# Kernel tuning notes

Hardware: AMD Instinct MI355X
Metric: run time of the kernel (lower is better)

## Reference

```python
import jax, jax.numpy as jnp
import numpy as np

NLAT, NLON = 361, 720
LMAX = NLAT               # equiangular grid: lmax = nlat
MMAX = NLON // 2 + 1      # mmax = nlon//2 + 1
B, C = 1, 128


def _precompute_legpoly(mmax, lmax, t, csphase=True):
    """Associated Legendre vandermonde P_l^m(cos t), orthonormal, inverse=True
    (norm factor 1 for 'ortho'). Shape [mmax, lmax, nlat]. Setup-time numpy only."""
    x = np.cos(t)
    nmax = max(mmax, lmax)
    vdm = np.zeros((nmax, nmax, len(x)))
    vdm[0, 0] = np.sqrt(1.0 / (4.0 * np.pi))
    for l in range(1, nmax):
        vdm[l - 1, l] = np.sqrt(2 * l + 1) * x * vdm[l - 1, l - 1]
        vdm[l, l] = np.sqrt((2 * l + 1) * (1 + x) * (1 - x) / (2 * l)) * vdm[l - 1, l - 1]
    for l in range(2, nmax):
        for m in range(l - 1):
            a = np.sqrt((2 * l - 1) / (l - m) * (2 * l + 1) / (l + m))
            b = np.sqrt((l + m - 1) / (l - m) * (2 * l + 1) / (2 * l - 3) * (l - m - 1) / (l + m))
            vdm[m, l] = a * x * vdm[m, l - 1] - b * vdm[m, l - 2]
    vdm = vdm[:mmax, :lmax]
    if csphase:
        vdm[1::2] *= -1.0  # Condon-Shortley phase on odd m
    return vdm


def setup_inputs() -> dict:
    key = jax.random.key(0)
    # spherical harmonic coefficients as real view: [B, C, lmax, mmax, 2]
    x_real = jax.random.normal(key, (B, C, LMAX, MMAX, 2), dtype=jnp.float32)
    # equiangular (Clenshaw-Curtiss) colatitudes, t = flip(arccos(cos(pi*j/(n-1))))
    t = np.pi * np.arange(NLAT) / (NLAT - 1)
    pct = jnp.asarray(_precompute_legpoly(MMAX, LMAX, t), dtype=jnp.float32)  # [mmax, lmax, nlat]
    return {"x_real": x_real, "pct": pct}


def reference(x_real, pct):
    # single-device case: comm sizes == 1, all distributed transposes are identity
    # and nlatpad == nlonpad == 0.
    # per-m triangular Legendre contraction over l (torch einsum '...lmr,mlk->...kmr')
    xs = jnp.einsum('bclmr,mlk->bckmr', x_real, pct)        # [B, C, nlat, mmax, 2]
    xc = jax.lax.complex(xs[..., 0], xs[..., 1])            # [B, C, nlat, mmax]
    # inverse real FFT along longitude, norm='forward' (no 1/n scaling on inverse)
    out = jnp.fft.irfft(xc, n=NLON, axis=-1, norm='forward')  # [B, C, nlat, nlon]
    return out.astype(x_real.dtype)
```

## Files before the change

kernel.cpp:

```cpp
#include <hip/hip_runtime.h>
#include <cstddef>

#define CC   128
#define LDIM 361
#define MDIM 361
#define KDIM 361
#define NLON 720
#define LP   384
#define KP   384
#define MRP  736
#define NP   768
#define CK   (CC*KDIM)
#define CR   (2*CC)

typedef __attribute__((ext_vector_type(8))) short short8;
typedef __attribute__((ext_vector_type(4))) float floatx4;

__device__ __forceinline__ unsigned short f2bf(float f) {
    union { float f; unsigned u; } v; v.f = f;
    unsigned u = v.u;
    u += 0x7fffu + ((u >> 16) & 1u);
    return (unsigned short)(u >> 16);
}

__device__ __forceinline__ void async_copy16(const void* g, void* l) {
    __builtin_amdgcn_global_load_lds(
        (const __attribute__((address_space(1))) void*)g,
        (__attribute__((address_space(3))) void*)l, 16, 0, 0);
}

__device__ __forceinline__ int xcd_swz(int id, int P) {
    int x = id & 7, g = id >> 3;
    int q = P >> 3, r = P & 7;
    int start = (x < r) ? x * (q + 1) : r * (q + 1) + (x - r) * q;
    return start + g;
}

__global__ void sht_gen_T(unsigned short* __restrict__ Tp) {
    int idx = blockIdx.x * 256 + threadIdx.x;
    if (idx >= NP * MRP) return;
    int n = idx / MRP, mr = idx - n * MRP;
    float v = 0.f;
    if (n < NLON && mr < 2 * MDIM) {
        int m = mr >> 1, im = mr & 1;
        if (m == 0)            v = im ? 0.f : 1.f;
        else if (m == MDIM-1)  v = im ? 0.f : ((n & 1) ? -1.f : 1.f);
        else {
            int ph = (m * n) % NLON;
            float ang = (float)ph * (float)(3.14159265358979323846 / 360.0);
            v = im ? (-2.f * sinf(ang)) : (2.f * cosf(ang));
        }
    }
    Tp[idx] = f2bf(v);
}

__global__ __launch_bounds__(256)
void sht_prep_x(const float* __restrict__ x, unsigned short* __restrict__ xA) {
    __shared__ float tp[2][64 * 33 + 4];
    const int mt = blockIdx.x;
    const int lt = blockIdx.y;
    const int c  = blockIdx.z;
    const int t  = threadIdx.x;

    #pragma unroll
    for (int u = 0; u < 8; ++u) {
        int p  = t + 256 * u;
        int li = p >> 5, mi = p & 31;
        int l = lt * 64 + li, m = mt * 32 + mi;
        float2 v = make_float2(0.f, 0.f);
        if (l < LDIM && m < MDIM)
            v = *(const float2*)(x + ((size_t)(c * LDIM + l) * MDIM + m) * 2);
        tp[0][li * 33 + mi] = v.x;
        tp[1][li * 33 + mi] = v.y;
    }
    __syncthreads();

    #pragma unroll
    for (int u = 0; u < 2; ++u) {
        int s  = t + 256 * u;
        int mi = s >> 4, rr = (s >> 3) & 1, lo = (s & 7) * 8;
        int m = mt * 32 + mi;
        if (m >= MDIM) continue;
        const float* pl = tp[rr];
        short8 h;
        #pragma unroll
        for (int e = 0; e < 8; ++e)
            h[e] = (short)f2bf(pl[(lo + e) * 33 + mi]);
        *(short8*)(xA + ((size_t)m * CR + 2 * c + rr) * LP + lt * 64 + lo) = h;
    }
}

__global__ __launch_bounds__(256)
void sht_prep_pct(const float* __restrict__ pct, unsigned short* __restrict__ pctT) {
    __shared__ float tile[32][129];
    const int m  = blockIdx.y;
    const int bx = blockIdx.x;
    const int kt = bx % 3, lt = bx / 3;
    const int l0 = lt * 32, k0 = kt * 128;
    const int t  = threadIdx.x;

    const int kk = t & 127, lw = t >> 7;
    #pragma unroll
    for (int u = 0; u < 16; ++u) {
        int li = lw + 2 * u;
        int l = l0 + li, k = k0 + kk;
        float v = 0.f;
        if (l < LDIM && k < KDIM)
            v = pct[((size_t)m * LDIM + l) * KDIM + k];
        tile[li][kk] = v;
    }
    __syncthreads();

    #pragma unroll
    for (int u = 0; u < 2; ++u) {
        int s = t + 256 * u;
        int ko = s >> 2, lo = (s & 3) * 8;
        short8 h;
        #pragma unroll
        for (int e = 0; e < 8; ++e)
            h[e] = (short)f2bf(tile[lo + e][ko]);
        *(short8*)(pctT + ((size_t)m * KP + k0 + ko) * LP + l0 + lo) = h;
    }
}

__global__ __launch_bounds__(512)
void sht_stageA2(const unsigned short* __restrict__ pctT, const unsigned short* __restrict__ xA,
                 unsigned short* __restrict__ xs) {
    __shared__ unsigned short As[128 * 32];
    __shared__ unsigned short Bs[384 * 32];

    const int p   = xcd_swz(blockIdx.x, 2 * MDIM);
    const int m   = p >> 1, ct = p & 1;
    const int c0  = ct * 128;
    const int t   = threadIdx.x;
    const int w   = t >> 6, L = t & 63;
    const int wr  = w & 1, wc = w >> 1;
    const int lane15 = L & 15, quad = L >> 4;
    const int arr = t >> 2, alq = t & 3;

    const unsigned short* xAm = xA + (size_t)m * CR * LP;
    const unsigned short* pTm = pctT + (size_t)m * KP * LP;

    floatx4 acc[4][6] = {};

    for (int kb = 0; kb < LP; kb += 32) {
        async_copy16(xAm + (size_t)(c0 + arr) * LP + kb + alq * 8,
                     As + (size_t)(w * 64) * 8);
        #pragma unroll
        for (int u = 0; u < 3; ++u) {
            int s = u * 512 + t;
            int rr = s >> 2, lq = s & 3;
            async_copy16(pTm + (size_t)rr * LP + kb + lq * 8,
                         Bs + (size_t)(u * 512 + w * 64) * 8);
        }
        __syncthreads();

        short8 af[4], bf[6];
        #pragma unroll
        for (int i = 0; i < 4; ++i)
            af[i] = *(const short8*)&As[((wr * 64 + i * 16 + lane15) * 4 + quad) * 8];
        #pragma unroll
        for (int j = 0; j < 6; ++j)
            bf[j] = *(const short8*)&Bs[((wc * 96 + j * 16 + lane15) * 4 + quad) * 8];
        #pragma unroll
        for (int i = 0; i < 4; ++i)
            #pragma unroll
            for (int j = 0; j < 6; ++j)
                acc[i][j] = __builtin_amdgcn_mfma_f32_16x16x32_bf16(af[i], bf[j], acc[i][j], 0, 0, 0);
        __syncthreads();
    }

    #pragma unroll
    for (int j = 0; j < 6; ++j) {
        int k = wc * 96 + j * 16 + lane15;
        if (k >= KDIM) continue;
        #pragma unroll
        for (int i = 0; i < 4; ++i) {
            #pragma unroll
            for (int eh = 0; eh < 2; ++eh) {
                int cr = c0 + wr * 64 + i * 16 + quad * 4 + eh * 2;
                int c  = cr >> 1;
                unsigned pack = (unsigned)f2bf(acc[i][j][eh * 2]) |
                                ((unsigned)f2bf(acc[i][j][eh * 2 + 1]) << 16);
                *(unsigned*)(xs + (size_t)(c * KDIM + k) * MRP + 2 * m) = pack;
            }
        }
    }
}

__global__ __launch_bounds__(256)
void sht_stageA(const float* __restrict__ pct, const unsigned short* __restrict__ xA,
                unsigned short* __restrict__ xs) {
    __shared__ unsigned short As[128 * 32];
    __shared__ unsigned short Bs[32 * 130];

    const int m   = blockIdx.y;
    const int ct  = blockIdx.x & 1;
    const int kt  = blockIdx.x >> 1;
    const int c0  = ct * 128;
    const int n0  = kt * 128;
    const int t   = threadIdx.x;
    const int w   = t >> 6, L = t & 63;
    const int wr  = w & 1, wc = w >> 1;
    const int lane15 = L & 15, quad = L >> 4;
    const int bl = t >> 3, bkq = t & 7;

    const unsigned short* xAm = xA + (size_t)m * CR * LP;
    const float* pctm = pct + (size_t)m * LDIM * KDIM;

    floatx4 acc[4][4] = {};

    for (int kb = 0; kb < LP; kb += 32) {
        #pragma unroll
        for (int i = 0; i < 2; ++i) {
            int s = w * 128 + i * 64 + L;
            int cr = s >> 2, lq = s & 3;
            async_copy16(xAm + (size_t)(c0 + cr) * LP + kb + lq * 8,
                         As + (size_t)(w * 128 + i * 64) * 8);
        }
        {
            int l = kb + bl;
            bool lok = (l < LDIM);
            const float* prow = pctm + (size_t)l * KDIM;
            #pragma unroll
            for (int u = 0; u < 4; ++u) {
                int kc = n0 + u * 32 + bkq * 4;
                float f0 = (lok && kc + 0 < KDIM) ? prow[kc + 0] : 0.f;
                float f1 = (lok && kc + 1 < KDIM) ? prow[kc + 1] : 0.f;
                float f2 = (lok && kc + 2 < KDIM) ? prow[kc + 2] : 0.f;
                float f3 = (lok && kc + 3 < KDIM) ? prow[kc + 3] : 0.f;
                unsigned* bp = (unsigned*)&Bs[bl * 130 + u * 32 + bkq * 4];
                bp[0] = (unsigned)f2bf(f0) | ((unsigned)f2bf(f1) << 16);
                bp[1] = (unsigned)f2bf(f2) | ((unsigned)f2bf(f3) << 16);
            }
        }
        __syncthreads();

        short8 af[4];
        #pragma unroll
        for (int i = 0; i < 4; ++i) {
            int row = wr * 64 + i * 16 + lane15;
            af[i] = *(const short8*)&As[(row * 4 + quad) * 8];
        }
        #pragma unroll
        for (int jf = 0; jf < 4; ++jf) {
            int col = wc * 64 + jf * 16 + lane15;
            short8 bf;
            #pragma unroll
            for (int j = 0; j < 8; ++j)
                bf[j] = (short)Bs[(quad * 8 + j) * 130 + col];
            #pragma unroll
            for (int i = 0; i < 4; ++i)
                acc[i][jf] = __builtin_amdgcn_mfma_f32_16x16x32_bf16(af[i], bf, acc[i][jf], 0, 0, 0);
        }
        __syncthreads();
    }

    #pragma unroll
    for (int i = 0; i < 4; ++i) {
        #pragma unroll
        for (int jf = 0; jf < 4; ++jf) {
            int k = n0 + wc * 64 + jf * 16 + lane15;
            if (k >= KDIM) continue;
            #pragma unroll
            for (int eh = 0; eh < 2; ++eh) {
                int cr = c0 + wr * 64 + i * 16 + quad * 4 + eh * 2;
                int c  = cr >> 1;
                unsigned pack = (unsigned)f2bf(acc[i][jf][eh * 2]) |
                                ((unsigned)f2bf(acc[i][jf][eh * 2 + 1]) << 16);
                *(unsigned*)(xs + (size_t)(c * KDIM + k) * MRP + 2 * m) = pack;
            }
        }
    }
}

__global__ __launch_bounds__(512)
void sht_stageB2(const unsigned short* __restrict__ xs, const unsigned short* __restrict__ Tp,
                 float* __restrict__ out) {
    __shared__ unsigned short As[128 * 32];
    __shared__ unsigned short Bs[384 * 32];

    const int p   = xcd_swz(blockIdx.x, 2 * MDIM);
    const int ckt = p >> 1, nt = p & 1;
    const int ck0 = ckt * 128, n0 = nt * 384;
    const int t   = threadIdx.x;
    const int w   = t >> 6, L = t & 63;
    const int wr  = w & 1, wc = w >> 1;
    const int lane15 = L & 15, quad = L >> 4;
    const int arr = t >> 2, alq = t & 3;

    floatx4 acc[4][6] = {};

    for (int kb = 0; kb < MRP; kb += 32) {
        async_copy16(xs + (size_t)(ck0 + arr) * MRP + kb + alq * 8,
                     As + (size_t)(w * 64) * 8);
        #pragma unroll
        for (int u = 0; u < 3; ++u) {
            int s = u * 512 + t;
            int rr = s >> 2, lq = s & 3;
            async_copy16(Tp + (size_t)(n0 + rr) * MRP + kb + lq * 8,
                         Bs + (size_t)(u * 512 + w * 64) * 8);
        }
        __syncthreads();

        short8 af[4], bf[6];
        #pragma unroll
        for (int i = 0; i < 4; ++i)
            af[i] = *(const short8*)&As[((wr * 64 + i * 16 + lane15) * 4 + quad) * 8];
        #pragma unroll
        for (int j = 0; j < 6; ++j)
            bf[j] = *(const short8*)&Bs[((wc * 96 + j * 16 + lane15) * 4 + quad) * 8];
        #pragma unroll
        for (int i = 0; i < 4; ++i)
            #pragma unroll
            for (int j = 0; j < 6; ++j)
                acc[i][j] = __builtin_amdgcn_mfma_f32_16x16x32_bf16(af[i], bf[j], acc[i][j], 0, 0, 0);
        __syncthreads();
    }

    #pragma unroll
    for (int i = 0; i < 4; ++i) {
        int ckr = ck0 + wr * 64 + i * 16 + quad * 4;
        #pragma unroll
        for (int j = 0; j < 6; ++j) {
            int jj = n0 + wc * 96 + j * 16 + lane15;
            if (jj >= NLON) continue;
            #pragma unroll
            for (int e = 0; e < 4; ++e)
                out[(size_t)(ckr + e) * NLON + jj] = acc[i][j][e];
        }
    }
}

extern "C" void kernel_launch(void* const* d_in, const int* in_sizes, int n_in,
                              void* d_out, int out_size, void* d_ws, size_t ws_size,
                              hipStream_t stream) {
    const float* x   = (const float*)d_in[0];
    const float* pct = (const float*)d_in[1];
    float* out = (float*)d_out;

    unsigned short* xs = (unsigned short*)d_ws;
    unsigned short* Tp = xs + (size_t)CK * MRP;
    unsigned short* xA = (unsigned short*)d_out;

    const size_t base_shorts = (size_t)CK * MRP + (size_t)NP * MRP;
    const size_t pctT_shorts = (size_t)MDIM * KP * LP;
    const bool fast = ws_size >= (base_shorts + pctT_shorts) * sizeof(unsigned short);

    sht_gen_T<<<(NP * MRP + 255) / 256, 256, 0, stream>>>(Tp);
    sht_prep_x<<<dim3(12, 6, 128), 256, 0, stream>>>(x, xA);
    if (fast) {
        unsigned short* pctT = Tp + (size_t)NP * MRP;
        sht_prep_pct<<<dim3(36, MDIM), 256, 0, stream>>>(pct, pctT);
        sht_stageA2<<<dim3(2 * MDIM), 512, 0, stream>>>(pctT, xA, xs);
    } else {
        sht_stageA<<<dim3(6, MDIM), 256, 0, stream>>>(pct, xA, xs);
    }
    sht_stageB2<<<dim3(2 * MDIM), 512, 0, stream>>>(xs, Tp, out);
}
```

Baseline: 676.0 us.

## Write stage-A output in m-major layout and transpose with a separate kernel

```diff
diff --git a/kernel.cpp b/kernel.cpp
--- a/kernel.cpp
+++ b/kernel.cpp
@@ -8,6 +8,7 @@
 #define NLON 720
 #define LP   384
 #define KP   384
+#define KTP  384
 #define MRP  736
 #define NP   768
 #define CK   (CC*KDIM)
@@ -56,7 +57,7 @@
 
 __global__ __launch_bounds__(256)
 void sht_prep_x(const float* __restrict__ x, unsigned short* __restrict__ xA) {
-    __shared__ float tp[2][64 * 33 + 4];
+    __shared__ float2 tile[64][33];
     const int mt = blockIdx.x;
     const int lt = blockIdx.y;
     const int c  = blockIdx.z;
@@ -70,8 +71,7 @@
         float2 v = make_float2(0.f, 0.f);
         if (l < LDIM && m < MDIM)
             v = *(const float2*)(x + ((size_t)(c * LDIM + l) * MDIM + m) * 2);
-        tp[0][li * 33 + mi] = v.x;
-        tp[1][li * 33 + mi] = v.y;
+        tile[li][mi] = v;
     }
     __syncthreads();
 
@@ -81,45 +81,139 @@
         int mi = s >> 4, rr = (s >> 3) & 1, lo = (s & 7) * 8;
         int m = mt * 32 + mi;
         if (m >= MDIM) continue;
-        const float* pl = tp[rr];
         short8 h;
         #pragma unroll
-        for (int e = 0; e < 8; ++e)
-            h[e] = (short)f2bf(pl[(lo + e) * 33 + mi]);
+        for (int e = 0; e < 8; ++e) {
+            float2 p = tile[lo + e][mi];
+            h[e] = (short)f2bf(rr ? p.y : p.x);
+        }
         *(short8*)(xA + ((size_t)m * CR + 2 * c + rr) * LP + lt * 64 + lo) = h;
     }
 }
 
 __global__ __launch_bounds__(256)
 void sht_prep_pct(const float* __restrict__ pct, unsigned short* __restrict__ pctT) {
-    __shared__ float tile[32][129];
+    __shared__ float tile[32][33];
     const int m  = blockIdx.y;
-    const int bx = blockIdx.x;
-    const int kt = bx % 3, lt = bx / 3;
-    const int l0 = lt * 32, k0 = kt * 128;
+    const int kt = blockIdx.x % 12;
+    const int lt = blockIdx.x / 12;
+    const int l0 = lt * 32, k0 = kt * 32;
     const int t  = threadIdx.x;
 
-    const int kk = t & 127, lw = t >> 7;
-    #pragma unroll
-    for (int u = 0; u < 16; ++u) {
-        int li = lw + 2 * u;
-        int l = l0 + li, k = k0 + kk;
+    const int ki = t & 31, lbase = t >> 5;
+    #pragma unroll
+    for (int u = 0; u < 4; ++u) {
+        int li = lbase + 8 * u;
+        int l = l0 + li, k = k0 + ki;
         float v = 0.f;
         if (l < LDIM && k < KDIM)
             v = pct[((size_t)m * LDIM + l) * KDIM + k];
-        tile[li][kk] = v;
+        tile[li][ki] = v;
     }
     __syncthreads();
 
-    #pragma unroll
-    for (int u = 0; u < 2; ++u) {
-        int s = t + 256 * u;
-        int ko = s >> 2, lo = (s & 3) * 8;
+    const int ko = t >> 3, lo = (t & 7) * 4;
+    unsigned pk0 = (unsigned)f2bf(tile[lo + 0][ko]) | ((unsigned)f2bf(tile[lo + 1][ko]) << 16);
+    unsigned pk1 = (unsigned)f2bf(tile[lo + 2][ko]) | ((unsigned)f2bf(tile[lo + 3][ko]) << 16);
+    unsigned* dst = (unsigned*)(pctT + ((size_t)m * KP + k0 + ko) * LP + l0 + lo);
+    dst[0] = pk0; dst[1] = pk1;
+}
+
+__global__ __launch_bounds__(512)
+void sht_stageA3(const unsigned short* __restrict__ pctT, const unsigned short* __restrict__ xA,
+                 unsigned short* __restrict__ xsT) {
+    __shared__ unsigned short As[128 * 32];
+    __shared__ unsigned short Bs[384 * 32];
+
+    const int p   = xcd_swz(blockIdx.x, 2 * MDIM);
+    const int m   = p >> 1, ct = p & 1;
+    const int c0  = ct * 128;
+    const int t   = threadIdx.x;
+    const int w   = t >> 6, L = t & 63;
+    const int wr  = w & 1, wc = w >> 1;
+    const int lane15 = L & 15, quad = L >> 4;
+    const int arr = t >> 2, alq = t & 3;
+
+    const unsigned short* xAm = xA + (size_t)m * CR * LP;
+    const unsigned short* pTm = pctT + (size_t)m * KP * LP;
+
+    floatx4 acc[4][6] = {};
+
+    for (int kb = 0; kb < LP; kb += 32) {
+        async_copy16(xAm + (size_t)(c0 + arr) * LP + kb + alq * 8,
+                     As + (size_t)(w * 64) * 8);
+        #pragma unroll
+        for (int u = 0; u < 3; ++u) {
+            int s = u * 512 + t;
+            int rr = s >> 2, lq = s & 3;
+            async_copy16(pTm + (size_t)rr * LP + kb + lq * 8,
+                         Bs + (size_t)(u * 512 + w * 64) * 8);
+        }
+        __syncthreads();
+
+        short8 af[4], bf[6];
+        #pragma unroll
+        for (int i = 0; i < 4; ++i)
+            af[i] = *(const short8*)&As[((wr * 64 + i * 16 + lane15) * 4 + quad) * 8];
+        #pragma unroll
+        for (int j = 0; j < 6; ++j)
+            bf[j] = *(const short8*)&Bs[((wc * 96 + j * 16 + lane15) * 4 + quad) * 8];
+        #pragma unroll
+        for (int i = 0; i < 4; ++i)
+            #pragma unroll
+            for (int j = 0; j < 6; ++j)
+                acc[i][j] = __builtin_amdgcn_mfma_f32_16x16x32_bf16(af[i], bf[j], acc[i][j], 0, 0, 0);
+        __syncthreads();
+    }
+
+    #pragma unroll
+    for (int i = 0; i < 4; ++i) {
+        #pragma unroll
+        for (int j = 0; j < 6; ++j) {
+            int k = wc * 96 + j * 16 + lane15;
+            #pragma unroll
+            for (int e = 0; e < 4; ++e) {
+                int cr = c0 + wr * 64 + i * 16 + quad * 4 + e;
+                xsT[((size_t)m * CR + cr) * KTP + k] = f2bf(acc[i][j][e]);
+            }
+        }
+    }
+}
+
+__global__ __launch_bounds__(256)
+void sht_xs_tr(const unsigned short* __restrict__ xsT, unsigned short* __restrict__ xs) {
+    __shared__ unsigned short tile[128 * 65];
+    const int c  = blockIdx.y;
+    const int bx = blockIdx.x;
+    const int mt = bx / 6, kt = bx % 6;
+    const int m0 = mt * 64, k0 = kt * 64;
+    const int t  = threadIdx.x;
+
+    #pragma unroll
+    for (int u = 0; u < 4; ++u) {
+        int q = t + 256 * u;
+        int rho = q >> 3, ko8 = q & 7;
+        int mi = rho >> 1, r = rho & 1;
+        int m = m0 + mi;
+        short8 v = {};
+        if (m < MDIM)
+            v = *(const short8*)(xsT + ((size_t)m * CR + 2 * c + r) * KTP + k0 + ko8 * 8);
+        *(short8*)&tile[rho * 65 + ko8 * 8] = v;
+    }
+    __syncthreads();
+
+    #pragma unroll
+    for (int u = 0; u < 4; ++u) {
+        int q = t + 256 * u;
+        int kk = q >> 4, mc = q & 15;
+        int k = k0 + kk;
+        int mr0 = 2 * m0 + mc * 8;
+        if (k >= KDIM || mr0 >= MRP) continue;
         short8 h;
         #pragma unroll
         for (int e = 0; e < 8; ++e)
-            h[e] = (short)f2bf(tile[lo + e][ko]);
-        *(short8*)(pctT + ((size_t)m * KP + k0 + ko) * LP + l0 + lo) = h;
+            h[e] = (short)tile[(mc * 8 + e) * 65 + kk];
+        *(short8*)(xs + (size_t)(c * KDIM + k) * MRP + mr0) = h;
     }
 }
 
@@ -345,13 +439,21 @@
 
     const size_t base_shorts = (size_t)CK * MRP + (size_t)NP * MRP;
     const size_t pctT_shorts = (size_t)MDIM * KP * LP;
-    const bool fast = ws_size >= (base_shorts + pctT_shorts) * sizeof(unsigned short);
+    const size_t xsT_shorts  = (size_t)MDIM * CR * KTP;
+    const bool fast1 = ws_size >= (base_shorts + pctT_shorts) * sizeof(unsigned short);
+    const bool fast2 = ws_size >= (base_shorts + pctT_shorts + xsT_shorts) * sizeof(unsigned short);
 
     sht_gen_T<<<(NP * MRP + 255) / 256, 256, 0, stream>>>(Tp);
     sht_prep_x<<<dim3(12, 6, 128), 256, 0, stream>>>(x, xA);
-    if (fast) {
+    if (fast2) {
         unsigned short* pctT = Tp + (size_t)NP * MRP;
-        sht_prep_pct<<<dim3(36, MDIM), 256, 0, stream>>>(pct, pctT);
+        unsigned short* xsT  = pctT + pctT_shorts;
+        sht_prep_pct<<<dim3(144, MDIM), 256, 0, stream>>>(pct, pctT);
+        sht_stageA3<<<dim3(2 * MDIM), 512, 0, stream>>>(pctT, xA, xsT);
+        sht_xs_tr<<<dim3(36, 128), 256, 0, stream>>>(xsT, xs);
+    } else if (fast1) {
+        unsigned short* pctT = Tp + (size_t)NP * MRP;
+        sht_prep_pct<<<dim3(144, MDIM), 256, 0, stream>>>(pct, pctT);
         sht_stageA2<<<dim3(2 * MDIM), 512, 0, stream>>>(pctT, xA, xs);
     } else {
         sht_stageA<<<dim3(6, MDIM), 256, 0, stream>>>(pct, xA, xs);
```

New measurement: 646.6 us. -4.4%, faster.
